# Kernel optimization log

Hardware: AMD Instinct MI355X
Metric: run time of the kernel (lower is better)

The kernel has to match this reference:

```python
import jax, jax.numpy as jnp
import numpy as np

N_EMBD = 2048
N_Q = 32
N_KV = 8
GROUP = N_Q // N_KV   # 4
HD = N_EMBD // N_Q    # 64
BASE = 10000.0
NEG_INF = -1e30


def _rope(x):
    """Rotate-half RoPE on last dim; positions 1..t along dim -2 (as in the
    original _build_cache which uses arange(1, seq_len+1))."""
    t, d = x.shape[-2], x.shape[-1]
    d2 = d // 2
    theta = 1.0 / (BASE ** (jnp.arange(0, d, 2, dtype=jnp.float32) / d))  # (d/2,)
    pos = jnp.arange(1, t + 1, dtype=jnp.float32)                          # (t,)
    ang = pos[:, None] * theta[None, :]                                    # (t, d/2)
    ang = jnp.concatenate([ang, ang], axis=-1)                             # (t, d)
    sin, cos = jnp.sin(ang), jnp.cos(ang)
    rot = jnp.concatenate([-x[..., d2:], x[..., :d2]], axis=-1)
    return x * cos + rot * sin


def setup_inputs() -> dict:
    key = jax.random.key(0)
    ks = jax.random.split(key, 5)
    b, t = 2, 1024
    s = 1.0 / np.sqrt(N_EMBD)
    return {
        "x": jax.random.normal(ks[0], (b, t, N_EMBD), dtype=jnp.float32),
        "wq": jax.random.normal(ks[1], (N_EMBD, N_EMBD), dtype=jnp.float32) * s,
        "bq": jnp.zeros((N_EMBD,), dtype=jnp.float32),
        "wk": jax.random.normal(ks[2], (N_EMBD, N_KV * HD), dtype=jnp.float32) * s,
        "bk": jnp.zeros((N_KV * HD,), dtype=jnp.float32),
        "wv": jax.random.normal(ks[3], (N_EMBD, N_KV * HD), dtype=jnp.float32) * s,
        "bv": jnp.zeros((N_KV * HD,), dtype=jnp.float32),
        "wo": jax.random.normal(ks[4], (N_EMBD, N_EMBD), dtype=jnp.float32) * s,
        "bo": jnp.zeros((N_EMBD,), dtype=jnp.float32),
    }


def reference(x, wq, bq, wk, bk, wv, bv, wo, bo):
    b, t, _ = x.shape
    q = x @ wq + bq                                   # (b, t, E)
    k = x @ wk + bk                                   # (b, t, NKV*HD)
    v = x @ wv + bv
    q = q.reshape(b, t, N_Q, HD).transpose(0, 2, 1, 3)        # (b, nq, t, d)
    q = q.reshape(b, N_KV, GROUP, t, HD)                      # (b, hkv, g, t, d)
    k = k.reshape(b, t, N_KV, HD).transpose(0, 2, 1, 3)       # (b, hkv, t, d)
    v = v.reshape(b, t, N_KV, HD).transpose(0, 2, 1, 3)
    q = _rope(q)
    k = _rope(k)
    scale = jnp.sqrt(jnp.float32(HD))
    att = jnp.einsum("bhgqd,bhkd->bhgqk", q, k) / scale       # (b, hkv, g, t, t)
    causal = jnp.tril(jnp.ones((t, t), dtype=bool))
    att = jnp.where(causal, att, NEG_INF)
    att = jax.nn.softmax(att, axis=-1)
    out = jnp.einsum("bhgqk,bhkd->bhgqd", att, v)             # (b, hkv, g, t, d)
    out = out.transpose(0, 3, 1, 2, 4).reshape(b, t, N_EMBD)  # (b, t, E)
    return out @ wo + bo
```

## Files before the change

### kernel.cpp

```cpp
#include <hip/hip_runtime.h>
#include <hip/hip_bf16.h>
#include <cstdint>


typedef __attribute__((ext_vector_type(8))) short short8;
typedef __attribute__((ext_vector_type(4))) short short4v;
typedef __attribute__((ext_vector_type(4))) float f32x4;

__device__ inline short f2b(float f) {
  union { float f; unsigned u; } v; v.f = f;
  unsigned r = v.u + 0x7fffu + ((v.u >> 16) & 1u);
  return (short)(r >> 16);
}

__device__ inline float exp2_fast(float x) {
  float r;
  asm("v_exp_f32 %0, %1" : "=v"(r) : "v"(x));
  return r;
}

__device__ inline void gl_lds16(const void* g, void* l) {
  __builtin_amdgcn_global_load_lds((const __attribute__((address_space(1))) void*)g,
                                   (__attribute__((address_space(3))) void*)l,
                                   16, 0, 0);
}

__global__ void cast_x_kernel(const float* __restrict__ x, short* __restrict__ xb, int n4) {
  int i = blockIdx.x * 256 + threadIdx.x;
  if (i >= n4) return;
  float4 v = ((const float4*)x)[i];
  short4v o; o.x = f2b(v.x); o.y = f2b(v.y); o.z = f2b(v.z); o.w = f2b(v.w);
  ((short4v*)xb)[i] = o;
}

__global__ void wtrans_kernel(const float* __restrict__ W, short* __restrict__ WT,
                              int N, int outRowOff, int outStride) {
  __shared__ float tile[64][65];
  const int nb = blockIdx.x * 64, kb = blockIdx.y * 64;
  const int tid = threadIdx.x;
  const int c = tid & 63, r0 = tid >> 6;
#pragma unroll
  for (int s = 0; s < 16; ++s) {
    int k = r0 + s * 4;
    tile[c][k] = W[(size_t)(kb + k) * N + nb + c];
  }
  __syncthreads();
#pragma unroll
  for (int s = 0; s < 16; ++s) {
    int n = r0 + s * 4;
    WT[(size_t)(outRowOff + nb + n) * outStride + kb + c] = f2b(tile[n][c]);
  }
}

__launch_bounds__(256, 3)
__global__ void gemm_qkv(const short* __restrict__ A, const short* __restrict__ BT,
                         const float* __restrict__ bq, const float* __restrict__ bk,
                         const float* __restrict__ bv,
                         short* __restrict__ Qb, short* __restrict__ Kb,
                         short* __restrict__ Vtd) {
  __shared__ __align__(16) short lA[128 * 32];
  __shared__ __align__(16) short lB[64 * 32];
  const int K = 2048;
  const int tid = threadIdx.x, lane = tid & 63, w = tid >> 6;
  const int q4 = lane >> 4, l15 = lane & 15;
  const int bn = blockIdx.x * 64, bm = blockIdx.y * 128;

  const short* Ag = A + (size_t)(bm + (tid >> 2)) * K + ((tid & 3) << 3);
  const short* Bg = BT + (size_t)(bn + (tid >> 2)) * K + ((tid & 3) << 3);
  short* lAw = lA + w * 512;
  short* lBw = lB + w * 512;

  f32x4 acc[2][4];
  const f32x4 fz = {0.f, 0.f, 0.f, 0.f};
#pragma unroll
  for (int i = 0; i < 2; ++i)
#pragma unroll
    for (int j = 0; j < 4; ++j) acc[i][j] = fz;

  for (int k0 = 0; k0 < K; k0 += 32) {
    gl_lds16(Ag + k0, lAw);
    gl_lds16(Ag + (size_t)64 * K + k0, lAw + 2048);
    gl_lds16(Bg + k0, lBw);
    __syncthreads();
    short8 af[2], bf[4];
#pragma unroll
    for (int mf = 0; mf < 2; ++mf) af[mf] = *(const short8*)(lA + (w * 32 + mf * 16 + l15) * 32 + q4 * 8);
#pragma unroll
    for (int nf = 0; nf < 4; ++nf) bf[nf] = *(const short8*)(lB + (nf * 16 + l15) * 32 + q4 * 8);
#pragma unroll
    for (int mf = 0; mf < 2; ++mf)
#pragma unroll
      for (int nf = 0; nf < 4; ++nf)
        acc[mf][nf] = __builtin_amdgcn_mfma_f32_16x16x32_bf16(af[mf], bf[nf], acc[mf][nf], 0, 0, 0);
    __syncthreads();
  }

  const float L2T = 0.4152410118609203f;
  const float theta_a = exp2_fast(-(float)l15 * L2T);
  const float theta_b = exp2_fast(-(float)(l15 + 16) * L2T);
  const float s2 = 0.18033688011112042f;

  if (bn < 2048) {
    const int h = bn >> 6;
    float bb0 = bq[bn + l15], bb1 = bq[bn + 16 + l15], bb2 = bq[bn + 32 + l15], bb3 = bq[bn + 48 + l15];
#pragma unroll
    for (int mf = 0; mf < 2; ++mf)
#pragma unroll
      for (int r = 0; r < 4; ++r) {
        int row = bm + w * 32 + mf * 16 + q4 * 4 + r;
        int batch = row >> 10, t = row & 1023;
        float pos = (float)(t + 1);
        float sa, ca, sb, cb;
        __sincosf(pos * theta_a, &sa, &ca);
        __sincosf(pos * theta_b, &sb, &cb);
        float x0 = acc[mf][0][r] + bb0, x2 = acc[mf][2][r] + bb2;
        float x1 = acc[mf][1][r] + bb1, x3 = acc[mf][3][r] + bb3;
        size_t base = ((size_t)(batch * 32 + h) * 1024 + t) * 64;
        Qb[base + l15]      = f2b((x0 * ca - x2 * sa) * s2);
        Qb[base + l15 + 32] = f2b((x2 * ca + x0 * sa) * s2);
        Qb[base + l15 + 16] = f2b((x1 * cb - x3 * sb) * s2);
        Qb[base + l15 + 48] = f2b((x3 * cb + x1 * sb) * s2);
      }
  } else if (bn < 2560) {
    const int co = bn - 2048;
    const int hkv = co >> 6;
    float bb0 = bk[co + l15], bb1 = bk[co + 16 + l15], bb2 = bk[co + 32 + l15], bb3 = bk[co + 48 + l15];
#pragma unroll
    for (int mf = 0; mf < 2; ++mf)
#pragma unroll
      for (int r = 0; r < 4; ++r) {
        int row = bm + w * 32 + mf * 16 + q4 * 4 + r;
        int batch = row >> 10, t = row & 1023;
        float pos = (float)(t + 1);
        float sa, ca, sb, cb;
        __sincosf(pos * theta_a, &sa, &ca);
        __sincosf(pos * theta_b, &sb, &cb);
        float x0 = acc[mf][0][r] + bb0, x2 = acc[mf][2][r] + bb2;
        float x1 = acc[mf][1][r] + bb1, x3 = acc[mf][3][r] + bb3;
        size_t base = (size_t)(batch * 8 + hkv) * 65536 + t * 32;
        Kb[base + l15]                = f2b(x0 * ca - x2 * sa);
        Kb[base + l15 + 16]           = f2b(x1 * cb - x3 * sb);
        Kb[base + 32768 + l15]        = f2b(x2 * ca + x0 * sa);
        Kb[base + 32768 + l15 + 16]   = f2b(x3 * cb + x1 * sb);
      }
  } else {
    const int co = bn - 2560;
    const int hkv = co >> 6;
    float bb[4];
#pragma unroll
    for (int nf = 0; nf < 4; ++nf) bb[nf] = bv[co + nf * 16 + l15];
#pragma unroll
    for (int mf = 0; mf < 2; ++mf)
#pragma unroll
      for (int r = 0; r < 4; ++r) {
        int row = bm + w * 32 + mf * 16 + q4 * 4 + r;
        int batch = row >> 10, t = row & 1023;
        size_t base = (size_t)(batch * 8 + hkv) * 65536 + (size_t)t * 64;
#pragma unroll
        for (int nf = 0; nf < 4; ++nf)
          Vtd[base + nf * 16 + l15] = f2b(acc[mf][nf][r] + bb[nf]);
      }
  }
}

__global__ void vtrans2_kernel(const short* __restrict__ Vtd, short* __restrict__ VTb) {
  __shared__ short tile[64][72];
  const int tt = blockIdx.x, h = blockIdx.y, b = blockIdx.z;
  const int tid = threadIdx.x;
  const size_t base = (size_t)(b * 8 + h) * 65536;
#pragma unroll
  for (int p = 0; p < 2; ++p) {
    int r = (tid >> 3) + p * 32;
    int c0 = (tid & 7) * 8;
    short8 v = *(const short8*)(Vtd + base + (size_t)(tt * 64 + r) * 64 + c0);
#pragma unroll
    for (int j = 0; j < 8; ++j) tile[c0 + j][r] = v[j];
  }
  __syncthreads();
  const int d = tid >> 2, ts = (tid & 3) * 8;
#pragma unroll
  for (int tc = 0; tc < 2; ++tc) {
    short8 v = *(const short8*)(&tile[d][tc * 32 + ts]);
    *(short8*)(VTb + base + (size_t)(tt * 2 + tc) * 2048 + d * 32 + ts) = v;
  }
}

#define PROW 72
__launch_bounds__(256, 3)
__global__ void attn5_kernel(const short* __restrict__ Qb, const short* __restrict__ Kb,
                             const short* __restrict__ VTb, short* __restrict__ AO) {
  __shared__ __align__(16) short lK[2][128 * 32];
  __shared__ __align__(16) short lVT[4][64 * 32];
  __shared__ __align__(16) short lP[4][2][16 * PROW];
  const int tid = threadIdx.x, lane = tid & 63, w = tid >> 6;
  const int q4 = lane >> 4, l15 = lane & 15;
  const int qt = (int)gridDim.x - 1 - (int)blockIdx.x;
  const int h = blockIdx.y, b = blockIdx.z;
  const int hkv = h >> 2;
  const int qb = qt * 128 + w * 32;
  const int kdiag = qb >> 6;
  const int ns = qt + 1;

  const short* Qg = Qb + (size_t)(b * 32 + h) * 65536;
  const short* Kg = Kb + (size_t)(b * 8 + hkv) * 65536;
  const short* Vg = VTb + (size_t)(b * 8 + hkv) * 65536;

  short8 qf[2][2];
#pragma unroll
  for (int mf = 0; mf < 2; ++mf) {
    const short* qr = Qg + (size_t)(qb + mf * 16 + l15) * 64 + q4 * 8;
    qf[mf][0] = *(const short8*)(qr);
    qf[mf][1] = *(const short8*)(qr + 32);
  }

  const f32x4 fz = {0.f, 0.f, 0.f, 0.f};
  f32x4 o[2][4], ol[2];
#pragma unroll
  for (int mf = 0; mf < 2; ++mf) {
    ol[mf] = fz;
#pragma unroll
    for (int i = 0; i < 4; ++i) o[mf][i] = fz;
  }
  short8 ones;
#pragma unroll
  for (int i = 0; i < 8; ++i) ones[i] = (short)0x3F80;

  for (int s = 0; s < ns; ++s) {
    {
      const short* Ksrc = Kg + (size_t)(s * 128 + (tid >> 2)) * 32 + (tid & 3) * 8;
      short* ldst = (short*)lK + w * 512;
      gl_lds16(Ksrc, ldst);
      gl_lds16(Ksrc + 64 * 32, ldst + 2048);
      gl_lds16(Ksrc + 32768, ldst + 4096);
      gl_lds16(Ksrc + 32768 + 64 * 32, ldst + 6144);
      const short* Vsrc = Vg + (size_t)(s * 4) * 2048 + tid * 8;
      short* vdst = (short*)lVT + w * 512;
#pragma unroll
      for (int c = 0; c < 4; ++c) gl_lds16(Vsrc + c * 2048, vdst + c * 2048);
    }
    __syncthreads();

#pragma unroll
    for (int ki = 0; ki < 2; ++ki) {
      const int ktg = s * 2 + ki;
      if (ktg <= kdiag) {
        short8 kf0[4], kf1[4];
#pragma unroll
        for (int nt = 0; nt < 4; ++nt) {
          kf0[nt] = *(const short8*)((short*)lK + (ki * 64 + nt * 16 + l15) * 32 + q4 * 8);
          kf1[nt] = *(const short8*)((short*)lK + 4096 + (ki * 64 + nt * 16 + l15) * 32 + q4 * 8);
        }
        const bool diag = (ktg == kdiag);
#pragma unroll
        for (int mf = 0; mf < 2; ++mf) {
          f32x4 sv[4];
#pragma unroll
          for (int nt = 0; nt < 4; ++nt) {
            f32x4 z = __builtin_amdgcn_mfma_f32_16x16x32_bf16(qf[mf][0], kf0[nt], fz, 0, 0, 0);
            sv[nt] = __builtin_amdgcn_mfma_f32_16x16x32_bf16(qf[mf][1], kf1[nt], z, 0, 0, 0);
          }
          if (diag) {
#pragma unroll
            for (int r = 0; r < 4; ++r) {
              const int qrow = qb + mf * 16 + q4 * 4 + r;
              const int col = ktg * 64 + l15;
#pragma unroll
              for (int nt = 0; nt < 4; ++nt)
                if (col + nt * 16 > qrow) sv[nt][r] = -1e30f;
            }
          }
          short* lPm = lP[w][mf];
#pragma unroll
          for (int r = 0; r < 4; ++r)
#pragma unroll
            for (int nt = 0; nt < 4; ++nt)
              lPm[(q4 * 4 + r) * PROW + nt * 16 + l15] = f2b(exp2_fast(sv[nt][r] - 16.f));
        }

        short8 vf0[4], vf1[4];
#pragma unroll
        for (int dt = 0; dt < 4; ++dt) {
          vf0[dt] = *(const short8*)((short*)lVT + (2 * ki) * 2048 + (dt * 16 + l15) * 32 + q4 * 8);
          vf1[dt] = *(const short8*)((short*)lVT + (2 * ki + 1) * 2048 + (dt * 16 + l15) * 32 + q4 * 8);
        }
#pragma unroll
        for (int mf = 0; mf < 2; ++mf) {
          const short* lPm = lP[w][mf];
          short8 pf0 = *(const short8*)(lPm + l15 * PROW + q4 * 8);
          short8 pf1 = *(const short8*)(lPm + l15 * PROW + 32 + q4 * 8);
          ol[mf] = __builtin_amdgcn_mfma_f32_16x16x32_bf16(pf0, ones, ol[mf], 0, 0, 0);
          ol[mf] = __builtin_amdgcn_mfma_f32_16x16x32_bf16(pf1, ones, ol[mf], 0, 0, 0);
#pragma unroll
          for (int dt = 0; dt < 4; ++dt) {
            o[mf][dt] = __builtin_amdgcn_mfma_f32_16x16x32_bf16(pf0, vf0[dt], o[mf][dt], 0, 0, 0);
            o[mf][dt] = __builtin_amdgcn_mfma_f32_16x16x32_bf16(pf1, vf1[dt], o[mf][dt], 0, 0, 0);
          }
        }
      }
    }
    __syncthreads();
  }

#pragma unroll
  for (int mf = 0; mf < 2; ++mf)
#pragma unroll
    for (int r = 0; r < 4; ++r) {
      float inv = __builtin_amdgcn_rcpf(ol[mf][r]);
      int row = qb + mf * 16 + q4 * 4 + r;
#pragma unroll
      for (int dt = 0; dt < 4; ++dt)
        AO[(size_t)(b * 1024 + row) * 2048 + h * 64 + dt * 16 + l15] = f2b(o[mf][dt][r] * inv);
    }
}

__launch_bounds__(256, 3)
__global__ void gemm_out(const short* __restrict__ A, const short* __restrict__ BT,
                         float* __restrict__ C, const float* __restrict__ bias,
                         int N, int K) {
  __shared__ __align__(16) short lA[128 * 32];
  __shared__ __align__(16) short lB[64 * 32];
  const int tid = threadIdx.x, lane = tid & 63, w = tid >> 6;
  const int q4 = lane >> 4, l15 = lane & 15;
  const int bn = blockIdx.x * 64, bm = blockIdx.y * 128;

  const short* Ag = A + (size_t)(bm + (tid >> 2)) * K + ((tid & 3) << 3);
  const short* Bg = BT + (size_t)(bn + (tid >> 2)) * K + ((tid & 3) << 3);
  short* lAw = lA + w * 512;
  short* lBw = lB + w * 512;

  f32x4 acc[2][4];
  const f32x4 fz = {0.f, 0.f, 0.f, 0.f};
#pragma unroll
  for (int i = 0; i < 2; ++i)
#pragma unroll
    for (int j = 0; j < 4; ++j) acc[i][j] = fz;

  for (int k0 = 0; k0 < K; k0 += 32) {
    gl_lds16(Ag + k0, lAw);
    gl_lds16(Ag + (size_t)64 * K + k0, lAw + 2048);
    gl_lds16(Bg + k0, lBw);
    __syncthreads();
    short8 af[2], bf[4];
#pragma unroll
    for (int mf = 0; mf < 2; ++mf) af[mf] = *(const short8*)(lA + (w * 32 + mf * 16 + l15) * 32 + q4 * 8);
#pragma unroll
    for (int nf = 0; nf < 4; ++nf) bf[nf] = *(const short8*)(lB + (nf * 16 + l15) * 32 + q4 * 8);
#pragma unroll
    for (int mf = 0; mf < 2; ++mf)
#pragma unroll
      for (int nf = 0; nf < 4; ++nf)
        acc[mf][nf] = __builtin_amdgcn_mfma_f32_16x16x32_bf16(af[mf], bf[nf], acc[mf][nf], 0, 0, 0);
    __syncthreads();
  }

#pragma unroll
  for (int mf = 0; mf < 2; ++mf)
#pragma unroll
    for (int nf = 0; nf < 4; ++nf) {
      int col = bn + nf * 16 + l15;
      float bb = bias[col];
#pragma unroll
      for (int r = 0; r < 4; ++r) {
        int row = bm + w * 32 + mf * 16 + q4 * 4 + r;
        C[(size_t)row * N + col] = acc[mf][nf][r] + bb;
      }
    }
}

extern "C" void kernel_launch(void* const* d_in, const int* in_sizes, int n_in,
                              void* d_out, int out_size, void* d_ws, size_t ws_size,
                              hipStream_t stream) {
  const float* x  = (const float*)d_in[0];
  const float* wq = (const float*)d_in[1];
  const float* bq = (const float*)d_in[2];
  const float* wk = (const float*)d_in[3];
  const float* bk = (const float*)d_in[4];
  const float* wv = (const float*)d_in[5];
  const float* bv = (const float*)d_in[6];
  const float* wo = (const float*)d_in[7];
  const float* bo = (const float*)d_in[8];
  float* out = (float*)d_out;
  const int B = in_sizes[0] / (1024 * 2048);
  const int M = B * 1024;

  char* ws = (char*)d_ws;
  size_t off = 0;
  auto alloc = [&](size_t bytes) -> char* {
    char* p = ws + off;
    off += (bytes + 255) & ~(size_t)255;
    return p;
  };
  short* xb    = (short*)alloc((size_t)M * 2048 * 2);
  short* WqkvT = (short*)alloc((size_t)3072 * 2048 * 2);
  short* woT   = (short*)alloc((size_t)2048 * 2048 * 2);
  short* Qb    = (short*)alloc((size_t)B * 32 * 1024 * 64 * 2);
  short* Kb    = (short*)alloc((size_t)B * 8 * 2 * 1024 * 32 * 2);
  short* Vtd   = (short*)alloc((size_t)B * 8 * 1024 * 64 * 2);
  short* VTb   = (short*)alloc((size_t)B * 8 * 32 * 64 * 32 * 2);
  short* AO    = (short*)alloc((size_t)M * 2048 * 2);

  cast_x_kernel<<<(M * 2048 / 4 + 255) / 256, 256, 0, stream>>>(x, xb, M * 2048 / 4);
  wtrans_kernel<<<dim3(32, 32), 256, 0, stream>>>(wq, WqkvT, 2048, 0, 2048);
  wtrans_kernel<<<dim3(8, 32), 256, 0, stream>>>(wk, WqkvT, 512, 2048, 2048);
  wtrans_kernel<<<dim3(8, 32), 256, 0, stream>>>(wv, WqkvT, 512, 2560, 2048);
  wtrans_kernel<<<dim3(32, 32), 256, 0, stream>>>(wo, woT, 2048, 0, 2048);
  gemm_qkv<<<dim3(48, M / 128), 256, 0, stream>>>(xb, WqkvT, bq, bk, bv, Qb, Kb, Vtd);
  vtrans2_kernel<<<dim3(16, 8, B), 256, 0, stream>>>(Vtd, VTb);
  attn5_kernel<<<dim3(8, 32, B), 256, 0, stream>>>(Qb, Kb, VTb, AO);
  gemm_out<<<dim3(32, M / 128), 256, 0, stream>>>(AO, woT, out, bo, 2048, 2048);
}
```

Measured before the change: 237.0 us.

## Double-buffer GEMM K-loop with BK=64 and merge weight transposes into one launch

```diff
diff --git a/kernel.cpp b/kernel.cpp
--- a/kernel.cpp
+++ b/kernel.cpp
@@ -33,10 +33,17 @@
   ((short4v*)xb)[i] = o;
 }
 
-__global__ void wtrans_kernel(const float* __restrict__ W, short* __restrict__ WT,
-                              int N, int outRowOff, int outStride) {
+__global__ void wtrans_all(const float* __restrict__ wq, const float* __restrict__ wk,
+                           const float* __restrict__ wv, const float* __restrict__ wo,
+                           short* __restrict__ WqkvT, short* __restrict__ woT) {
   __shared__ float tile[64][65];
-  const int nb = blockIdx.x * 64, kb = blockIdx.y * 64;
+  const int bx = blockIdx.x;
+  const float* W; short* WT; int N, off, nb;
+  if (bx < 32)      { W = wq; WT = WqkvT; N = 2048; off = 0;    nb = bx * 64; }
+  else if (bx < 40) { W = wk; WT = WqkvT; N = 512;  off = 2048; nb = (bx - 32) * 64; }
+  else if (bx < 48) { W = wv; WT = WqkvT; N = 512;  off = 2560; nb = (bx - 40) * 64; }
+  else              { W = wo; WT = woT;   N = 2048; off = 0;    nb = (bx - 48) * 64; }
+  const int kb = blockIdx.y * 64;
   const int tid = threadIdx.x;
   const int c = tid & 63, r0 = tid >> 6;
 #pragma unroll
@@ -48,7 +55,48 @@
 #pragma unroll
   for (int s = 0; s < 16; ++s) {
     int n = r0 + s * 4;
-    WT[(size_t)(outRowOff + nb + n) * outStride + kb + c] = f2b(tile[n][c]);
+    WT[(size_t)(off + nb + n) * 2048 + kb + c] = f2b(tile[n][c]);
+  }
+}
+
+__device__ __forceinline__ void gemm_loop_bk64(const short* __restrict__ Ag,
+                                               const short* __restrict__ Bg,
+                                               short* lA, short* lB,
+                                               int w, int l15, int q4,
+                                               f32x4 acc[2][4]) {
+  const int K = 2048, NS = 32;
+  auto stage = [&](int s, int d) {
+    const short* As = Ag + s * 64;
+    const short* Bs = Bg + s * 64;
+    short* a = lA + d * 8192 + w * 512;
+    gl_lds16(As, a);
+    gl_lds16(As + 64 * K, a + 2048);
+    gl_lds16(As + 32, a + 4096);
+    gl_lds16(As + 64 * K + 32, a + 6144);
+    short* bp = lB + d * 4096 + w * 512;
+    gl_lds16(Bs, bp);
+    gl_lds16(Bs + 32, bp + 2048);
+  };
+  stage(0, 0);
+  for (int s = 0; s < NS; ++s) {
+    const int d = s & 1;
+    __syncthreads();
+    if (s + 1 < NS) stage(s + 1, d ^ 1);
+#pragma unroll
+    for (int ks = 0; ks < 2; ++ks) {
+      const short* ap = lA + d * 8192 + ks * 4096;
+      const short* bp = lB + d * 4096 + ks * 2048;
+      short8 af[2], bf[4];
+#pragma unroll
+      for (int mf = 0; mf < 2; ++mf) af[mf] = *(const short8*)(ap + (w * 32 + mf * 16 + l15) * 32 + q4 * 8);
+#pragma unroll
+      for (int nf = 0; nf < 4; ++nf) bf[nf] = *(const short8*)(bp + (nf * 16 + l15) * 32 + q4 * 8);
+#pragma unroll
+      for (int mf = 0; mf < 2; ++mf)
+#pragma unroll
+        for (int nf = 0; nf < 4; ++nf)
+          acc[mf][nf] = __builtin_amdgcn_mfma_f32_16x16x32_bf16(af[mf], bf[nf], acc[mf][nf], 0, 0, 0);
+    }
   }
 }
 
@@ -58,8 +106,8 @@
                          const float* __restrict__ bv,
                          short* __restrict__ Qb, short* __restrict__ Kb,
                          short* __restrict__ Vtd) {
-  __shared__ __align__(16) short lA[128 * 32];
-  __shared__ __align__(16) short lB[64 * 32];
+  __shared__ __align__(16) short lA[16384];
+  __shared__ __align__(16) short lB[8192];
   const int K = 2048;
   const int tid = threadIdx.x, lane = tid & 63, w = tid >> 6;
   const int q4 = lane >> 4, l15 = lane & 15;
@@ -67,8 +115,6 @@
 
   const short* Ag = A + (size_t)(bm + (tid >> 2)) * K + ((tid & 3) << 3);
   const short* Bg = BT + (size_t)(bn + (tid >> 2)) * K + ((tid & 3) << 3);
-  short* lAw = lA + w * 512;
-  short* lBw = lB + w * 512;
 
   f32x4 acc[2][4];
   const f32x4 fz = {0.f, 0.f, 0.f, 0.f};
@@ -77,23 +123,7 @@
 #pragma unroll
     for (int j = 0; j < 4; ++j) acc[i][j] = fz;
 
-  for (int k0 = 0; k0 < K; k0 += 32) {
-    gl_lds16(Ag + k0, lAw);
-    gl_lds16(Ag + (size_t)64 * K + k0, lAw + 2048);
-    gl_lds16(Bg + k0, lBw);
-    __syncthreads();
-    short8 af[2], bf[4];
-#pragma unroll
-    for (int mf = 0; mf < 2; ++mf) af[mf] = *(const short8*)(lA + (w * 32 + mf * 16 + l15) * 32 + q4 * 8);
-#pragma unroll
-    for (int nf = 0; nf < 4; ++nf) bf[nf] = *(const short8*)(lB + (nf * 16 + l15) * 32 + q4 * 8);
-#pragma unroll
-    for (int mf = 0; mf < 2; ++mf)
-#pragma unroll
-      for (int nf = 0; nf < 4; ++nf)
-        acc[mf][nf] = __builtin_amdgcn_mfma_f32_16x16x32_bf16(af[mf], bf[nf], acc[mf][nf], 0, 0, 0);
-    __syncthreads();
-  }
+  gemm_loop_bk64(Ag, Bg, lA, lB, w, l15, q4, acc);
 
   const float L2T = 0.4152410118609203f;
   const float theta_a = exp2_fast(-(float)l15 * L2T);
@@ -138,10 +168,10 @@
         float x0 = acc[mf][0][r] + bb0, x2 = acc[mf][2][r] + bb2;
         float x1 = acc[mf][1][r] + bb1, x3 = acc[mf][3][r] + bb3;
         size_t base = (size_t)(batch * 8 + hkv) * 65536 + t * 32;
-        Kb[base + l15]                = f2b(x0 * ca - x2 * sa);
-        Kb[base + l15 + 16]           = f2b(x1 * cb - x3 * sb);
-        Kb[base + 32768 + l15]        = f2b(x2 * ca + x0 * sa);
-        Kb[base + 32768 + l15 + 16]   = f2b(x3 * cb + x1 * sb);
+        Kb[base + l15]              = f2b(x0 * ca - x2 * sa);
+        Kb[base + l15 + 16]         = f2b(x1 * cb - x3 * sb);
+        Kb[base + 32768 + l15]      = f2b(x2 * ca + x0 * sa);
+        Kb[base + 32768 + l15 + 16] = f2b(x3 * cb + x1 * sb);
       }
   } else {
     const int co = bn - 2560;
@@ -317,16 +347,14 @@
 __global__ void gemm_out(const short* __restrict__ A, const short* __restrict__ BT,
                          float* __restrict__ C, const float* __restrict__ bias,
                          int N, int K) {
-  __shared__ __align__(16) short lA[128 * 32];
-  __shared__ __align__(16) short lB[64 * 32];
+  __shared__ __align__(16) short lA[16384];
+  __shared__ __align__(16) short lB[8192];
   const int tid = threadIdx.x, lane = tid & 63, w = tid >> 6;
   const int q4 = lane >> 4, l15 = lane & 15;
   const int bn = blockIdx.x * 64, bm = blockIdx.y * 128;
 
   const short* Ag = A + (size_t)(bm + (tid >> 2)) * K + ((tid & 3) << 3);
   const short* Bg = BT + (size_t)(bn + (tid >> 2)) * K + ((tid & 3) << 3);
-  short* lAw = lA + w * 512;
-  short* lBw = lB + w * 512;
 
   f32x4 acc[2][4];
   const f32x4 fz = {0.f, 0.f, 0.f, 0.f};
@@ -335,23 +363,7 @@
 #pragma unroll
     for (int j = 0; j < 4; ++j) acc[i][j] = fz;
 
-  for (int k0 = 0; k0 < K; k0 += 32) {
-    gl_lds16(Ag + k0, lAw);
-    gl_lds16(Ag + (size_t)64 * K + k0, lAw + 2048);
-    gl_lds16(Bg + k0, lBw);
-    __syncthreads();
-    short8 af[2], bf[4];
-#pragma unroll
-    for (int mf = 0; mf < 2; ++mf) af[mf] = *(const short8*)(lA + (w * 32 + mf * 16 + l15) * 32 + q4 * 8);
-#pragma unroll
-    for (int nf = 0; nf < 4; ++nf) bf[nf] = *(const short8*)(lB + (nf * 16 + l15) * 32 + q4 * 8);
-#pragma unroll
-    for (int mf = 0; mf < 2; ++mf)
-#pragma unroll
-      for (int nf = 0; nf < 4; ++nf)
-        acc[mf][nf] = __builtin_amdgcn_mfma_f32_16x16x32_bf16(af[mf], bf[nf], acc[mf][nf], 0, 0, 0);
-    __syncthreads();
-  }
+  gemm_loop_bk64(Ag, Bg, lA, lB, w, l15, q4, acc);
 
 #pragma unroll
   for (int mf = 0; mf < 2; ++mf)
@@ -400,10 +412,7 @@
   short* AO    = (short*)alloc((size_t)M * 2048 * 2);
 
   cast_x_kernel<<<(M * 2048 / 4 + 255) / 256, 256, 0, stream>>>(x, xb, M * 2048 / 4);
-  wtrans_kernel<<<dim3(32, 32), 256, 0, stream>>>(wq, WqkvT, 2048, 0, 2048);
-  wtrans_kernel<<<dim3(8, 32), 256, 0, stream>>>(wk, WqkvT, 512, 2048, 2048);
-  wtrans_kernel<<<dim3(8, 32), 256, 0, stream>>>(wv, WqkvT, 512, 2560, 2048);
-  wtrans_kernel<<<dim3(32, 32), 256, 0, stream>>>(wo, woT, 2048, 0, 2048);
+  wtrans_all<<<dim3(80, 32), 256, 0, stream>>>(wq, wk, wv, wo, WqkvT, woT);
   gemm_qkv<<<dim3(48, M / 128), 256, 0, stream>>>(xb, WqkvT, bq, bk, bv, Qb, Kb, Vtd);
   vtrans2_kernel<<<dim3(16, 8, B), 256, 0, stream>>>(Vtd, VTb);
   attn5_kernel<<<dim3(8, 32, B), 256, 0, stream>>>(Qb, Kb, VTb, AO);
```

Result: faster. 209.7 us (-11.5%).
